# Kernel tuning notes

Measured on AMD Instinct MI355X. Metric: run time of the kernel, lower is better.

## Reference

```python
import jax, jax.numpy as jnp
import numpy as np

B, S, T = 1024, 1024, 32  # batch, seq_len, num_tags


def setup_inputs() -> dict:
    key = jax.random.key(0)
    k1, k2, k3, k4 = jax.random.split(key, 4)
    logits = jax.random.normal(k1, (B, S, T), dtype=jnp.float32)
    transitions = jax.random.normal(k2, (T, T), dtype=jnp.float32)
    tags = jax.random.randint(k3, (B, S), 0, T)
    lengths = jax.random.randint(k4, (B,), 1, S + 1)
    return {"logits": logits, "transitions": transitions, "tags": tags, "lengths": lengths}


def _forward_alg(logits, transitions):
    # viterbi_0 = logits[:, 0, :]; then for t>=1:
    # v_next[b, j] = logsumexp_i(v[b, i] + trans[i, j]) + logits[b, t, j]
    v0 = logits[:, 0, :]  # (B, T)
    emits = jnp.swapaxes(logits[:, 1:, :], 0, 1)  # (S-1, B, T)

    def step(v, emit_t):
        v_next = jax.nn.logsumexp(v[:, :, None] + transitions[None, :, :], axis=1) + emit_t
        return v_next, None

    v_final, _ = jax.lax.scan(step, v0, emits)
    return jax.nn.logsumexp(v_final, axis=1)  # (B,)


def _score_sentence(logits, transitions, tags, lengths):
    # emission scores of gold tags, masked to t < length (note: original ignores
    # lengths in the forward algorithm but uses them here, faithfully reproduced)
    emit = jnp.take_along_axis(logits, tags[:, :, None], axis=2)[..., 0]  # (B, S)
    pos = jnp.arange(S)
    emit_mask = (pos[None, :] < lengths[:, None]).astype(logits.dtype)
    score = jnp.sum(emit * emit_mask, axis=1)
    # transition scores trans[tags[t-1], tags[t]] for 1 <= t < length
    trans_sc = transitions[tags[:, :-1], tags[:, 1:]]  # (B, S-1)
    trans_mask = (pos[None, 1:] < lengths[:, None]).astype(logits.dtype)
    score = score + jnp.sum(trans_sc * trans_mask, axis=1)
    return score  # (B,)


def reference(logits, transitions, tags, lengths):
    log_z = _forward_alg(logits, transitions)
    gold = _score_sentence(logits, transitions, tags, lengths)
    return jnp.mean(log_z - gold)
```

## Files before the change

### kernel.cpp

```cpp
#include <hip/hip_runtime.h>

#define NB 1024
#define NS 1024
#define NT 32
#define L2E 1.44269504088896340736f
#define LN2 0.69314718055994530942f

typedef short        bfrag  __attribute__((ext_vector_type(8)));
typedef float        cfrag  __attribute__((ext_vector_type(16)));
typedef __bf16       bf16x2 __attribute__((ext_vector_type(2)));
typedef float        f32x8  __attribute__((ext_vector_type(8)));
typedef float        f32x4  __attribute__((ext_vector_type(4)));
typedef float        f32x2  __attribute__((ext_vector_type(2)));
typedef unsigned int u32;
typedef unsigned int u32x4  __attribute__((ext_vector_type(4)));

__device__ __forceinline__ float fexp2(float x){ return __builtin_amdgcn_exp2f(x); }
__device__ __forceinline__ float flog2(float x){ return __builtin_amdgcn_logf(x); }

__device__ __forceinline__ u32 pkbf_rne(float a, float b){
    f32x2 t; t.x = a; t.y = b;
    return __builtin_bit_cast(u32, __builtin_convertvector(t, bf16x2));
}
__device__ __forceinline__ u32 pkbf_t(float a, float b){
    return __builtin_amdgcn_perm(__builtin_bit_cast(u32, b),
                                 __builtin_bit_cast(u32, a), 0x07060302u);
}
__device__ __forceinline__ int exref(float ref){
    u32 xb = __builtin_bit_cast(u32, ref);
    u32 xf = __builtin_amdgcn_readfirstlane(xb);
    int ex = (int)((xf >> 23) & 0xFFu) - 127;
    return ex < -120 ? -120 : (ex > 120 ? 120 : ex);
}

__device__ __forceinline__ int rho(int k){
    int bb = (k >> 2) & 3;
    return (bb == 1 || bb == 2) ? (k ^ 12) : k;
}

template<int N> struct ic { static constexpr int value = N; };
union accu { cfrag c; f32x2 p[8]; };
union e8u  { f32x8 v; f32x2 p[4]; };

#define MFMA2(Au, Bu, C) __builtin_amdgcn_mfma_f32_32x32x16_bf16( \
    __builtin_bit_cast(bfrag, Au), __builtin_bit_cast(bfrag, Bu), (C), 0, 0, 0)

__global__ __launch_bounds__(128, 6) void crf_chunk(
    const float* __restrict__ logits, const float* __restrict__ trans,
    const int* __restrict__ tags, const int* __restrict__ lens,
    u32* __restrict__ wmat, float* __restrict__ woff,
    float* __restrict__ gpart, float* __restrict__ outz)
{
    const int tid = threadIdx.x;
    const int wv  = tid >> 6, lt = tid & 63;
    const int m   = lt & 31,  h  = lt >> 5;
    const int bc  = blockIdx.x * 2 + wv;
    const int b   = bc >> 3,  c  = bc & 7;

    if (blockIdx.x == 0 && tid == 0) *outz = 0.0f;

    const float* base = logits + (size_t)b * NS * NT;
    const int    len  = lens[b];
    const int    tb   = b * NS;

    e8u Et0, Et1;
    #pragma unroll
    for (int j = 0; j < 8; j++){
        Et0.v[j] = fexp2(L2E * trans[rho(     8*h + j)*NT + m]);
        Et1.v[j] = fexp2(L2E * trans[rho(16 + 8*h + j)*NT + m]);
    }

    u32x4 B0v, B1v;
    #pragma unroll
    for (int d = 0; d < 4; d++){
        int k0 = 8*h + 2*d;      u32 v = 0;
        if (rho(k0)     == m) v |= 0x3F80u;
        if (rho(k0 + 1) == m) v |= 0x3F800000u;
        B0v[d] = v;
        int k1 = 16 + 8*h + 2*d; v = 0;
        if (rho(k1)     == m) v |= 0x3F80u;
        if (rho(k1 + 1) == m) v |= 0x3F800000u;
        B1v[d] = v;
    }

    cfrag zacc;
    #pragma unroll
    for (int q = 0; q < 16; q++) zacc[q] = 0.0f;

    int   offi = 0;
    float exf  = 0.0f;
    const int tbeg = c*128 + 1;

    float eA[8], eB[8];

    auto issue = [&](float (&e)[8], int k){
        const int t0 = tbeg + k*8;
        #pragma unroll
        for (int i = 0; i < 8; i++){
            int t = t0 + i; t = t > (NS-1) ? (NS-1) : t;
            e[i] = base[t*NT + m];
        }
    };

    auto procN = [&](float (&e)[8], bool defer, auto nstc){
        constexpr int NST = decltype(nstc)::value;
        #pragma unroll
        for (int i = 0; i < NST; i++){
            float s = (i == 0) ? fexp2(fmaf(L2E, e[0], -exf))
                               : fexp2(L2E * e[i]);
            f32x2 s2; s2.x = s; s2.y = s;

            u32x4 A0p, A1p;
            {
                f32x2 r0 = Et0.p[0]*s2, r1 = Et0.p[1]*s2;
                f32x2 r2 = Et0.p[2]*s2, r3 = Et0.p[3]*s2;
                A0p[0] = pkbf_t(r0.x, r0.y); A0p[1] = pkbf_t(r1.x, r1.y);
                A0p[2] = pkbf_t(r2.x, r2.y); A0p[3] = pkbf_t(r3.x, r3.y);
                f32x2 q0 = Et1.p[0]*s2, q1 = Et1.p[1]*s2;
                f32x2 q2 = Et1.p[2]*s2, q3 = Et1.p[3]*s2;
                A1p[0] = pkbf_t(q0.x, q0.y); A1p[1] = pkbf_t(q1.x, q1.y);
                A1p[2] = pkbf_t(q2.x, q2.y); A1p[3] = pkbf_t(q3.x, q3.y);
            }

            accu acc;
            acc.c = MFMA2(A0p, B0v, zacc);
            acc.c = MFMA2(A1p, B1v, acc.c);

            if (i == 7 && defer){
                int ex = exref(fmaxf(acc.c[0], acc.c[8]));
                offi += ex;
                exf = (float)ex;
            }

            B0v[0] = pkbf_t(acc.c[0],  acc.c[1]);  B0v[1] = pkbf_t(acc.c[2],  acc.c[3]);
            B0v[2] = pkbf_t(acc.c[4],  acc.c[5]);  B0v[3] = pkbf_t(acc.c[6],  acc.c[7]);
            B1v[0] = pkbf_t(acc.c[8],  acc.c[9]);  B1v[1] = pkbf_t(acc.c[10], acc.c[11]);
            B1v[2] = pkbf_t(acc.c[12], acc.c[13]); B1v[3] = pkbf_t(acc.c[14], acc.c[15]);
        }
    };

    issue(eA, 0);
    #pragma unroll 1
    for (int k = 0; k < 14; k += 2){
        issue(eB, k + 1);
        procN(eA, true, ic<8>{});
        issue(eA, k + 2);
        procN(eB, true, ic<8>{});
    }
    issue(eB, 15);
    procN(eA, true, ic<8>{});
    if (c != 7) procN(eB, false, ic<8>{});
    else        procN(eB, false, ic<7>{});

    {
        u32* wp = wmat + (size_t)bc * 512 + (size_t)lt * 8;
        *(u32x4*)(wp)     = B0v;
        *(u32x4*)(wp + 4) = B1v;
    }
    if (lt == 0) woff[bc] = (float)offi;

    {
        const int t1 = tbeg + 2*lt;
        const int t2 = t1 + 1;
        const int i2 = t2 > (NS-1) ? (NS-1) : t2;
        const int g0 = tags[tb + t1 - 1];
        const int g1 = tags[tb + t1];
        const int g2 = tags[tb + i2];
        float gg = 0.0f;
        if (t1 < len) gg += base[t1*NT + g1] + trans[g0*NT + g1];
        if (t2 < len) gg += base[t2*NT + g2] + trans[g1*NT + g2];
        #pragma unroll
        for (int d = 1; d < 64; d <<= 1) gg += __shfl_xor(gg, d, 64);
        if (lt == 0){
            if (c == 0) gg += base[tags[tb]];
            gpart[bc] = gg;
        }
    }
}

__global__ __launch_bounds__(256) void crf_combine(
    const float* __restrict__ logits,
    const u32* __restrict__ wmat, const float* __restrict__ woff,
    const float* __restrict__ gpart, float* __restrict__ out)
{
    const int tid = threadIdx.x;
    const int wv  = tid >> 6, lt = tid & 63;
    const int m   = lt & 31,  h  = lt >> 5;
    const int b   = blockIdx.x * 4 + wv;
    const float* base = logits + (size_t)b * NS * NT;

    uint4 mf[16];
    const u32* wb = wmat + (size_t)b * 8 * 512 + (size_t)lt * 8;
    #pragma unroll
    for (int j = 0; j < 8; j++){
        mf[2*j]     = *(const uint4*)(wb + j*512);
        mf[2*j + 1] = *(const uint4*)(wb + j*512 + 4);
    }

    float4 gp0 = ((const float4*)(gpart + b*8))[0];
    float4 gp1 = ((const float4*)(gpart + b*8))[1];
    const float gold = (gp0.x + gp0.y) + (gp0.z + gp0.w)
                     + (gp1.x + gp1.y) + (gp1.z + gp1.w);

    float voff = 0.0f;
    #pragma unroll
    for (int cc = 0; cc < 8; cc++) voff += woff[b*8 + cc];

    u32x4 S0, S1;
    #pragma unroll
    for (int d = 0; d < 4; d++){
        int k0 = 8*h + 2*d;      u32 v = 0;
        if (rho(k0)     == m) v |= 0x3F80u;
        if (rho(k0 + 1) == m) v |= 0x3F800000u;
        S0[d] = v;
        int k1 = 16 + 8*h + 2*d; v = 0;
        if (rho(k1)     == m) v |= 0x3F80u;
        if (rho(k1 + 1) == m) v |= 0x3F800000u;
        S1[d] = v;
    }

    cfrag zacc;
    #pragma unroll
    for (int q = 0; q < 16; q++) zacc[q] = 0.0f;

    #pragma unroll
    for (int j = 7; j >= 0; j--){
        accu acc;
        acc.c = MFMA2(mf[2*j],     S0, zacc);
        acc.c = MFMA2(mf[2*j + 1], S1, acc.c);

        float mx = acc.c[0];
        #pragma unroll
        for (int q = 1; q < 16; q++) mx = fmaxf(mx, acc.c[q]);
        #pragma unroll
        for (int d = 1; d < 64; d <<= 1) mx = fmaxf(mx, __shfl_xor(mx, d, 64));
        int ex = exref(mx);
        float sc = __builtin_bit_cast(float, (u32)(127 - ex) << 23);
        #pragma unroll
        for (int q = 0; q < 16; q++) acc.c[q] *= sc;
        voff += (float)ex;

        S0[0] = pkbf_t(acc.c[0],  acc.c[1]);  S0[1] = pkbf_t(acc.c[2],  acc.c[3]);
        S0[2] = pkbf_t(acc.c[4],  acc.c[5]);  S0[3] = pkbf_t(acc.c[6],  acc.c[7]);
        S1[0] = pkbf_t(acc.c[8],  acc.c[9]);  S1[1] = pkbf_t(acc.c[10], acc.c[11]);
        S1[2] = pkbf_t(acc.c[12], acc.c[13]); S1[3] = pkbf_t(acc.c[14], acc.c[15]);
    }

    u32x4 V0, V1;
    #pragma unroll
    for (int d = 0; d < 4; d++){
        int k0 = 8*h + 2*d;
        V0[d] = pkbf_rne(fexp2(L2E * base[rho(k0)]), fexp2(L2E * base[rho(k0+1)]));
        int k1 = 16 + 8*h + 2*d;
        V1[d] = pkbf_rne(fexp2(L2E * base[rho(k1)]), fexp2(L2E * base[rho(k1+1)]));
    }

    accu fin;
    fin.c = MFMA2(S0, V0, zacc);
    fin.c = MFMA2(S1, V1, fin.c);

    float s = 0.0f;
    #pragma unroll
    for (int q = 0; q < 16; q++) s += fin.c[q];
    s += __shfl_xor(s, 32, 64);

    if (lt == 0){
        float logz = LN2 * (voff + flog2(s));
        atomicAdd(out, (logz - gold) * (1.0f / (float)NB));
    }
}

extern "C" void kernel_launch(void* const* d_in, const int* in_sizes, int n_in,
                              void* d_out, int out_size, void* d_ws, size_t ws_size,
                              hipStream_t stream) {
    const float* logits = (const float*)d_in[0];
    const float* trans  = (const float*)d_in[1];
    const int*   tags   = (const int*)d_in[2];
    const int*   lens   = (const int*)d_in[3];

    u32*   wmat  = (u32*)d_ws;
    float* woff  = (float*)((char*)d_ws + 16u*1024u*1024u);
    float* gpart = woff + 8192;

    crf_chunk  <<<4096, 128, 0, stream>>>(logits, trans, tags, lens,
                                          wmat, woff, gpart, (float*)d_out);
    crf_combine<<< 256, 256, 0, stream>>>(logits, wmat, woff, gpart,
                                          (float*)d_out);
}
```

Measured before the change: 258.5 us.

## Pair timesteps into independent two-step factors to shorten serial MFMA chain

Instead of one dependent MFMA pair per timestep, each pair of timesteps is first combined into a standalone two-step transfer matrix (built from LDS-staged emission exponentials and transitions), computed off the critical path. The running state then multiplies by one factor per two steps, with produce and apply interleaved so the independent MFMAs hide latency. Renormalisation now rescales the accumulator explicitly instead of folding an offset into the next exponent. This adds LDS traffic, more registers (launch bounds lowered from 6 to 4 blocks), and an extra bf16 rounding in each combined factor.

```diff
diff --git a/kernel.cpp b/kernel.cpp
--- a/kernel.cpp
+++ b/kernel.cpp
@@ -38,24 +38,26 @@
     return (bb == 1 || bb == 2) ? (k ^ 12) : k;
 }
 
-template<int N> struct ic { static constexpr int value = N; };
 union accu { cfrag c; f32x2 p[8]; };
 union e8u  { f32x8 v; f32x2 p[4]; };
 
 #define MFMA2(Au, Bu, C) __builtin_amdgcn_mfma_f32_32x32x16_bf16( \
     __builtin_bit_cast(bfrag, Au), __builtin_bit_cast(bfrag, Bu), (C), 0, 0, 0)
 
-__global__ __launch_bounds__(128, 6) void crf_chunk(
+__global__ __launch_bounds__(128, 4) void crf_chunk(
     const float* __restrict__ logits, const float* __restrict__ trans,
     const int* __restrict__ tags, const int* __restrict__ lens,
     u32* __restrict__ wmat, float* __restrict__ woff,
     float* __restrict__ gpart, float* __restrict__ outz)
 {
+    __shared__ __align__(16) float dscall[2 * 256];
+
     const int tid = threadIdx.x;
     const int wv  = tid >> 6, lt = tid & 63;
     const int m   = lt & 31,  h  = lt >> 5;
     const int bc  = blockIdx.x * 2 + wv;
     const int b   = bc >> 3,  c  = bc & 7;
+    float* dsc = dscall + wv * 256;
 
     if (blockIdx.x == 0 && tid == 0) *outz = 0.0f;
 
@@ -63,35 +65,41 @@
     const int    len  = lens[b];
     const int    tb   = b * NS;
 
-    e8u Et0, Et1;
+    e8u Et0, Et1, EB0, EB1;
     #pragma unroll
     for (int j = 0; j < 8; j++){
         Et0.v[j] = fexp2(L2E * trans[rho(     8*h + j)*NT + m]);
         Et1.v[j] = fexp2(L2E * trans[rho(16 + 8*h + j)*NT + m]);
-    }
-
-    u32x4 B0v, B1v;
+        EB0.v[j] = fexp2(L2E * trans[m*NT + rho(     8*h + j)]);
+        EB1.v[j] = fexp2(L2E * trans[m*NT + rho(16 + 8*h + j)]);
+    }
+    const int ra0 = rho(8*h + 0), ra1 = rho(8*h + 2);
+    const int ra2 = rho(8*h + 4), ra3 = rho(8*h + 6);
+    const int rb0 = rho(16 + 8*h + 0), rb1 = rho(16 + 8*h + 2);
+    const int rb2 = rho(16 + 8*h + 4), rb3 = rho(16 + 8*h + 6);
+
+    u32x4 M0, M1;
     #pragma unroll
     for (int d = 0; d < 4; d++){
         int k0 = 8*h + 2*d;      u32 v = 0;
         if (rho(k0)     == m) v |= 0x3F80u;
         if (rho(k0 + 1) == m) v |= 0x3F800000u;
-        B0v[d] = v;
+        M0[d] = v;
         int k1 = 16 + 8*h + 2*d; v = 0;
         if (rho(k1)     == m) v |= 0x3F80u;
         if (rho(k1 + 1) == m) v |= 0x3F800000u;
-        B1v[d] = v;
+        M1[d] = v;
     }
 
     cfrag zacc;
     #pragma unroll
     for (int q = 0; q < 16; q++) zacc[q] = 0.0f;
 
-    int   offi = 0;
-    float exf  = 0.0f;
+    int offi = 0;
     const int tbeg = c*128 + 1;
 
     float eA[8], eB[8];
+    u32x4 Fa0, Fa1, Fb0, Fb1;
 
     auto issue = [&](float (&e)[8], int k){
         const int t0 = tbeg + k*8;
@@ -101,61 +109,128 @@
             e[i] = base[t*NT + m];
         }
     };
-
-    auto procN = [&](float (&e)[8], bool defer, auto nstc){
-        constexpr int NST = decltype(nstc)::value;
-        #pragma unroll
-        for (int i = 0; i < NST; i++){
-            float s = (i == 0) ? fexp2(fmaf(L2E, e[0], -exf))
-                               : fexp2(L2E * e[i]);
-            f32x2 s2; s2.x = s; s2.y = s;
-
-            u32x4 A0p, A1p;
-            {
-                f32x2 r0 = Et0.p[0]*s2, r1 = Et0.p[1]*s2;
-                f32x2 r2 = Et0.p[2]*s2, r3 = Et0.p[3]*s2;
-                A0p[0] = pkbf_t(r0.x, r0.y); A0p[1] = pkbf_t(r1.x, r1.y);
-                A0p[2] = pkbf_t(r2.x, r2.y); A0p[3] = pkbf_t(r3.x, r3.y);
-                f32x2 q0 = Et1.p[0]*s2, q1 = Et1.p[1]*s2;
-                f32x2 q2 = Et1.p[2]*s2, q3 = Et1.p[3]*s2;
-                A1p[0] = pkbf_t(q0.x, q0.y); A1p[1] = pkbf_t(q1.x, q1.y);
-                A1p[2] = pkbf_t(q2.x, q2.y); A1p[3] = pkbf_t(q3.x, q3.y);
-            }
-
-            accu acc;
-            acc.c = MFMA2(A0p, B0v, zacc);
-            acc.c = MFMA2(A1p, B1v, acc.c);
-
-            if (i == 7 && defer){
-                int ex = exref(fmaxf(acc.c[0], acc.c[8]));
-                offi += ex;
-                exf = (float)ex;
-            }
-
-            B0v[0] = pkbf_t(acc.c[0],  acc.c[1]);  B0v[1] = pkbf_t(acc.c[2],  acc.c[3]);
-            B0v[2] = pkbf_t(acc.c[4],  acc.c[5]);  B0v[3] = pkbf_t(acc.c[6],  acc.c[7]);
-            B1v[0] = pkbf_t(acc.c[8],  acc.c[9]);  B1v[1] = pkbf_t(acc.c[10], acc.c[11]);
-            B1v[2] = pkbf_t(acc.c[12], acc.c[13]); B1v[3] = pkbf_t(acc.c[14], acc.c[15]);
+    auto commitE = [&](float (&e)[8], int k){
+        if (h == 0){
+            float* sp = dsc + (k & 1)*128 + m;
+            sp[0]  = fexp2(L2E * e[0]);
+            sp[32] = fexp2(L2E * e[2]);
+            sp[64] = fexp2(L2E * e[4]);
+            sp[96] = fexp2(L2E * e[6]);
         }
     };
 
-    issue(eA, 0);
+    auto produceF = [&](float (&e)[8], int k, int i, u32x4 &F0, u32x4 &F1){
+        const float* db = dsc + (k & 1)*128 + i*32;
+        f32x2 ca0 = *(const f32x2*)(db + ra0);
+        f32x2 ca1 = *(const f32x2*)(db + ra1);
+        f32x2 ca2 = *(const f32x2*)(db + ra2);
+        f32x2 ca3 = *(const f32x2*)(db + ra3);
+        f32x2 cb0 = *(const f32x2*)(db + rb0);
+        f32x2 cb1 = *(const f32x2*)(db + rb1);
+        f32x2 cb2 = *(const f32x2*)(db + rb2);
+        f32x2 cb3 = *(const f32x2*)(db + rb3);
+        float s = fexp2(L2E * e[2*i + 1]);
+        f32x2 s2; s2.x = s; s2.y = s;
+
+        u32x4 Ae0, Ae1, Bo0, Bo1;
+        f32x2 t;
+        t = EB0.p[0]*ca0; Ae0[0] = pkbf_t(t.x, t.y);
+        t = EB0.p[1]*ca1; Ae0[1] = pkbf_t(t.x, t.y);
+        t = EB0.p[2]*ca2; Ae0[2] = pkbf_t(t.x, t.y);
+        t = EB0.p[3]*ca3; Ae0[3] = pkbf_t(t.x, t.y);
+        t = EB1.p[0]*cb0; Ae1[0] = pkbf_t(t.x, t.y);
+        t = EB1.p[1]*cb1; Ae1[1] = pkbf_t(t.x, t.y);
+        t = EB1.p[2]*cb2; Ae1[2] = pkbf_t(t.x, t.y);
+        t = EB1.p[3]*cb3; Ae1[3] = pkbf_t(t.x, t.y);
+        t = Et0.p[0]*s2;  Bo0[0] = pkbf_t(t.x, t.y);
+        t = Et0.p[1]*s2;  Bo0[1] = pkbf_t(t.x, t.y);
+        t = Et0.p[2]*s2;  Bo0[2] = pkbf_t(t.x, t.y);
+        t = Et0.p[3]*s2;  Bo0[3] = pkbf_t(t.x, t.y);
+        t = Et1.p[0]*s2;  Bo1[0] = pkbf_t(t.x, t.y);
+        t = Et1.p[1]*s2;  Bo1[1] = pkbf_t(t.x, t.y);
+        t = Et1.p[2]*s2;  Bo1[2] = pkbf_t(t.x, t.y);
+        t = Et1.p[3]*s2;  Bo1[3] = pkbf_t(t.x, t.y);
+
+        accu r;
+        r.c = MFMA2(Ae0, Bo0, zacc);
+        r.c = MFMA2(Ae1, Bo1, r.c);
+        F0[0] = pkbf_t(r.c[0],  r.c[1]);  F0[1] = pkbf_t(r.c[2],  r.c[3]);
+        F0[2] = pkbf_t(r.c[4],  r.c[5]);  F0[3] = pkbf_t(r.c[6],  r.c[7]);
+        F1[0] = pkbf_t(r.c[8],  r.c[9]);  F1[1] = pkbf_t(r.c[10], r.c[11]);
+        F1[2] = pkbf_t(r.c[12], r.c[13]); F1[3] = pkbf_t(r.c[14], r.c[15]);
+    };
+
+    auto applyF = [&](u32x4 &F0, u32x4 &F1, bool rn){
+        accu acc;
+        acc.c = MFMA2(F0, M0, zacc);
+        acc.c = MFMA2(F1, M1, acc.c);
+        if (rn){
+            int ex = exref(fmaxf(acc.c[0], acc.c[8]));
+            offi += ex;
+            f32x2 s2; s2.x = s2.y = __builtin_bit_cast(float, (u32)(127 - ex) << 23);
+            #pragma unroll
+            for (int q = 0; q < 8; q++) acc.p[q] *= s2;
+        }
+        M0[0] = pkbf_t(acc.c[0],  acc.c[1]);  M0[1] = pkbf_t(acc.c[2],  acc.c[3]);
+        M0[2] = pkbf_t(acc.c[4],  acc.c[5]);  M0[3] = pkbf_t(acc.c[6],  acc.c[7]);
+        M1[0] = pkbf_t(acc.c[8],  acc.c[9]);  M1[1] = pkbf_t(acc.c[10], acc.c[11]);
+        M1[2] = pkbf_t(acc.c[12], acc.c[13]); M1[3] = pkbf_t(acc.c[14], acc.c[15]);
+    };
+
+    auto grp = [&](float (&ec)[8], float (&en)[8], int k){
+        produceF(ec, k, 1, Fb0, Fb1);  applyF(Fa0, Fa1, false);
+        produceF(ec, k, 2, Fa0, Fa1);  applyF(Fb0, Fb1, false);
+        produceF(ec, k, 3, Fb0, Fb1);  applyF(Fa0, Fa1, false);
+        commitE(en, k + 1);
+        produceF(en, k + 1, 0, Fa0, Fa1);
+        applyF(Fb0, Fb1, true);
+    };
+
+    issue(eA, 0); commitE(eA, 0);
+    produceF(eA, 0, 0, Fa0, Fa1);
     #pragma unroll 1
     for (int k = 0; k < 14; k += 2){
         issue(eB, k + 1);
-        procN(eA, true, ic<8>{});
+        grp(eA, eB, k);
         issue(eA, k + 2);
-        procN(eB, true, ic<8>{});
+        grp(eB, eA, k + 1);
     }
     issue(eB, 15);
-    procN(eA, true, ic<8>{});
-    if (c != 7) procN(eB, false, ic<8>{});
-    else        procN(eB, false, ic<7>{});
+    grp(eA, eB, 14);
+
+    if (c != 7){
+        produceF(eB, 15, 1, Fb0, Fb1); applyF(Fa0, Fa1, false);
+        produceF(eB, 15, 2, Fa0, Fa1); applyF(Fb0, Fb1, false);
+        produceF(eB, 15, 3, Fb0, Fb1); applyF(Fa0, Fa1, false);
+        applyF(Fb0, Fb1, false);
+    } else {
+        produceF(eB, 15, 1, Fb0, Fb1); applyF(Fa0, Fa1, false);
+        produceF(eB, 15, 2, Fa0, Fa1); applyF(Fb0, Fb1, false);
+        applyF(Fa0, Fa1, false);
+        float s = fexp2(L2E * eB[6]);
+        f32x2 s2; s2.x = s; s2.y = s;
+        u32x4 As0, As1; f32x2 t;
+        t = Et0.p[0]*s2; As0[0] = pkbf_t(t.x, t.y);
+        t = Et0.p[1]*s2; As0[1] = pkbf_t(t.x, t.y);
+        t = Et0.p[2]*s2; As0[2] = pkbf_t(t.x, t.y);
+        t = Et0.p[3]*s2; As0[3] = pkbf_t(t.x, t.y);
+        t = Et1.p[0]*s2; As1[0] = pkbf_t(t.x, t.y);
+        t = Et1.p[1]*s2; As1[1] = pkbf_t(t.x, t.y);
+        t = Et1.p[2]*s2; As1[2] = pkbf_t(t.x, t.y);
+        t = Et1.p[3]*s2; As1[3] = pkbf_t(t.x, t.y);
+        accu acc;
+        acc.c = MFMA2(As0, M0, zacc);
+        acc.c = MFMA2(As1, M1, acc.c);
+        M0[0] = pkbf_t(acc.c[0],  acc.c[1]);  M0[1] = pkbf_t(acc.c[2],  acc.c[3]);
+        M0[2] = pkbf_t(acc.c[4],  acc.c[5]);  M0[3] = pkbf_t(acc.c[6],  acc.c[7]);
+        M1[0] = pkbf_t(acc.c[8],  acc.c[9]);  M1[1] = pkbf_t(acc.c[10], acc.c[11]);
+        M1[2] = pkbf_t(acc.c[12], acc.c[13]); M1[3] = pkbf_t(acc.c[14], acc.c[15]);
+    }
 
     {
         u32* wp = wmat + (size_t)bc * 512 + (size_t)lt * 8;
-        *(u32x4*)(wp)     = B0v;
-        *(u32x4*)(wp + 4) = B1v;
+        *(u32x4*)(wp)     = M0;
+        *(u32x4*)(wp + 4) = M1;
     }
     if (lt == 0) woff[bc] = (float)offi;
 
```

After: 301.0 us. 16.4% more time.
